# Kernel tuning notes

Hardware: AMD Instinct MI355X
Metric: run time of the kernel (lower is better)

The kernel has to match this reference:

```python
import jax, jax.numpy as jnp
import numpy as np

B, D, R = 4096, 1024, 256
DT = 0.01
DT_SCALE = 1.0

# Yoshida 4th-order coefficients
_W1 = 1.0 / (2.0 - 2.0 ** (1.0 / 3.0))
_W0 = -(2.0 ** (1.0 / 3.0)) / (2.0 - 2.0 ** (1.0 / 3.0))
C1 = _W1 / 2.0
C2 = (_W0 + _W1) / 2.0
C3 = C2
C4 = C1
D1 = _W1
D2 = _W0
D3 = _W1


def setup_inputs() -> dict:
    key = jax.random.key(0)
    k1, k2, k3, k4, k5 = jax.random.split(key, 5)
    x = jax.random.normal(k1, (B, D), dtype=jnp.float32)
    v = jax.random.normal(k2, (B, D), dtype=jnp.float32)
    force = jax.random.normal(k3, (B, D), dtype=jnp.float32)
    # low-rank christoffel factors, scaled for numerical stability
    U = jax.random.normal(k4, (R, D), dtype=jnp.float32) * (1.0 / np.sqrt(D))
    W = jax.random.normal(k5, (D, R), dtype=jnp.float32) * (1.0 / np.sqrt(R))
    return {"x": x, "v": v, "force": force, "U": U, "W": W}


def _christoffel(tv, tx, U, W):
    # Gamma(v) = W @ (U v)^2  (low-rank quadratic form; x unused, matching
    # the gfn yoshida_fused(U, W) signature)
    h = jnp.einsum("rd,bd->br", U, tv)  # [B, R]
    return jnp.einsum("dr,br->bd", W, h * h)  # [B, D]


def reference(x, v, force, U, W):
    dt = DT * DT_SCALE

    def acceleration(tx, tv):
        return -_christoffel(tv, tx, U, W) + force

    x1 = x + C1 * dt * v
    v1 = v + D1 * dt * acceleration(x1, v)
    x2 = x1 + C2 * dt * v1
    v2 = v1 + D2 * dt * acceleration(x2, v1)
    x3 = x2 + C3 * dt * v2
    v3 = v2 + D3 * dt * acceleration(x3, v2)
    x_final = x3 + C4 * dt * v3
    return (x_final, v3)
```

## Files before the change

### kernel.cpp

```cpp
#include <hip/hip_runtime.h>
#include <hip/hip_bf16.h>


#define BSZ 4096
#define DD 1024
#define RR 256

typedef unsigned short ushort_t;
typedef __attribute__((ext_vector_type(8))) short short8;
typedef __attribute__((ext_vector_type(4))) float f32x4;

__device__ inline ushort_t f2b(float x) {
    union { float f; unsigned int u; } c;
    c.f = x;
    unsigned int lsb = (c.u >> 16) & 1u;
    return (ushort_t)((c.u + 0x7fffu + lsb) >> 16);
}

__global__ __launch_bounds__(256) void pack_uw_kernel(
    const float* __restrict__ U, const float* __restrict__ W,
    ushort_t* __restrict__ Upk, ushort_t* __restrict__ Wpk)
{
    const int g = blockIdx.x * 256 + threadIdx.x;
    const float* src;
    ushort_t* dst;
    if (g < 32768) {
        const int l = g & 63;
        const int kt = (g >> 6) & 31, nt = g >> 11;
        src = U + (size_t)(nt * 16 + (l & 15)) * DD + kt * 32 + (l >> 4) * 8;
        dst = Upk + (size_t)g * 8;
    } else {
        const int g2 = g - 32768;
        const int l = g2 & 63;
        const int kt = (g2 >> 6) & 7, dtile = g2 >> 9;
        src = W + (size_t)(dtile * 16 + (l & 15)) * RR + kt * 32 + (l >> 4) * 8;
        dst = Wpk + (size_t)g2 * 8;
    }
    const float4 a = *reinterpret_cast<const float4*>(src);
    const float4 b = *reinterpret_cast<const float4*>(src + 4);
    ushort_t t[8] = {f2b(a.x), f2b(a.y), f2b(a.z), f2b(a.w),
                     f2b(b.x), f2b(b.y), f2b(b.z), f2b(b.w)};
    *reinterpret_cast<short8*>(dst) = *reinterpret_cast<short8*>(t);
}

__global__ __launch_bounds__(1024) void yoshida_fused_kernel(
    const float* __restrict__ x_in,
    const float* __restrict__ v_in,
    const float* __restrict__ force,
    const ushort_t* __restrict__ Upk,
    const ushort_t* __restrict__ Wpk,
    float* __restrict__ x_out,
    float* __restrict__ v_out)
{
    __shared__ __align__(16) ushort_t vS[16][1032];
    __shared__ __align__(16) ushort_t H2S[16][264];

    const int tid = threadIdx.x;
    const int w = tid >> 6;
    const int l = tid & 63;
    const int m = l & 15;
    const int q = l >> 4;
    const int b0 = blockIdx.x * 16;
    const int d0 = w * 64;

    constexpr double CBRT2 = 1.2599210498948731647672106072782;
    constexpr double W1c = 1.0 / (2.0 - CBRT2);
    constexpr double W0c = -CBRT2 * W1c;
    constexpr double DTd = 0.01 * 1.0;
    const float dcoef[3] = {(float)(W1c * DTd), (float)(W0c * DTd), (float)(W1c * DTd)};
    const float xcoef[3] = {(float)((W0c + W1c) * 0.5), (float)((W0c + W1c) * 0.5),
                            (float)(W1c * 0.5)};
    const float c1  = (float)(W1c * 0.5);
    const float dtf = (float)DTd;

    float vreg[16], xacc[16], freg[16];
    #pragma unroll
    for (int t = 0; t < 4; ++t)
        #pragma unroll
        for (int i = 0; i < 4; ++i) {
            const size_t gidx = (size_t)(b0 + q * 4 + i) * DD + d0 + t * 16 + m;
            const float vv = v_in[gidx];
            vreg[t * 4 + i] = vv;
            xacc[t * 4 + i] = c1 * vv;
            freg[t * 4 + i] = force[gidx];
        }

    {
        const int row = tid >> 6;
        const int col = (tid & 63) * 16;
        const float* sp = v_in + (size_t)(b0 + row) * DD + col;
        const float4 f0 = *reinterpret_cast<const float4*>(sp);
        const float4 f1 = *reinterpret_cast<const float4*>(sp + 4);
        const float4 f2 = *reinterpret_cast<const float4*>(sp + 8);
        const float4 f3 = *reinterpret_cast<const float4*>(sp + 12);
        ushort_t tmp[16] = {f2b(f0.x), f2b(f0.y), f2b(f0.z), f2b(f0.w),
                            f2b(f1.x), f2b(f1.y), f2b(f1.z), f2b(f1.w),
                            f2b(f2.x), f2b(f2.y), f2b(f2.z), f2b(f2.w),
                            f2b(f3.x), f2b(f3.y), f2b(f3.z), f2b(f3.w)};
        *reinterpret_cast<short8*>(&vS[row][col])     = *reinterpret_cast<short8*>(&tmp[0]);
        *reinterpret_cast<short8*>(&vS[row][col + 8]) = *reinterpret_cast<short8*>(&tmp[8]);
    }

    const ushort_t* up = Upk + (size_t)(w * 16384 + l * 8);
    const ushort_t* wp = Wpk + (size_t)(w * 16384 + l * 8);

    short8 ub[4];
    #pragma unroll
    for (int p = 0; p < 4; ++p)
        ub[p] = *reinterpret_cast<const short8*>(up + (size_t)p * 512);

    #pragma unroll
    for (int s = 0; s < 3; ++s) {
        __syncthreads();

        f32x4 a0 = {0.f, 0.f, 0.f, 0.f}, a1 = {0.f, 0.f, 0.f, 0.f};
        #pragma unroll
        for (int kt = 0; kt < 32; ++kt) {
            const short8 b = ub[kt & 3];
            if (kt < 28)
                ub[kt & 3] = *reinterpret_cast<const short8*>(up + (size_t)(kt + 4) * 512);
            const short8 a = *reinterpret_cast<const short8*>(&vS[m][kt * 32 + q * 8]);
            if (kt & 1) a1 = __builtin_amdgcn_mfma_f32_16x16x32_bf16(a, b, a1, 0, 0, 0);
            else        a0 = __builtin_amdgcn_mfma_f32_16x16x32_bf16(a, b, a0, 0, 0, 0);
        }
        #pragma unroll
        for (int i = 0; i < 4; ++i) {
            const float h = a0[i] + a1[i];
            H2S[q * 4 + i][w * 16 + m] = f2b(h * h);
        }

        short8 wb[4];
        #pragma unroll
        for (int t = 0; t < 4; ++t)
            wb[t] = *reinterpret_cast<const short8*>(wp + (size_t)(t * 8) * 512);
        __syncthreads();

        f32x4 accB[4];
        #pragma unroll
        for (int t = 0; t < 4; ++t) accB[t] = (f32x4){0.f, 0.f, 0.f, 0.f};
        #pragma unroll
        for (int kt = 0; kt < 8; ++kt) {
            const short8 a = *reinterpret_cast<const short8*>(&H2S[m][kt * 32 + q * 8]);
            #pragma unroll
            for (int t = 0; t < 4; ++t) {
                const short8 b = wb[t];
                if (kt < 7)
                    wb[t] = *reinterpret_cast<const short8*>(wp + (size_t)(t * 8 + kt + 1) * 512);
                accB[t] = __builtin_amdgcn_mfma_f32_16x16x32_bf16(a, b, accB[t], 0, 0, 0);
            }
        }

        const float ddt = dcoef[s], cx = xcoef[s];
        #pragma unroll
        for (int t = 0; t < 4; ++t)
            #pragma unroll
            for (int i = 0; i < 4; ++i) {
                const float vn = vreg[t * 4 + i] + ddt * (freg[t * 4 + i] - accB[t][i]);
                vreg[t * 4 + i] = vn;
                xacc[t * 4 + i] += cx * vn;
                vS[q * 4 + i][d0 + t * 16 + m] = f2b(vn);
            }

        if (s < 2) {
            #pragma unroll
            for (int p = 0; p < 4; ++p)
                ub[p] = *reinterpret_cast<const short8*>(up + (size_t)p * 512);
        }
    }

    #pragma unroll
    for (int t = 0; t < 4; ++t)
        #pragma unroll
        for (int i = 0; i < 4; ++i) {
            const size_t g = (size_t)(b0 + q * 4 + i) * DD + d0 + t * 16 + m;
            x_out[g] = x_in[g] + dtf * xacc[t * 4 + i];
            v_out[g] = vreg[t * 4 + i];
        }
}

extern "C" void kernel_launch(void* const* d_in, const int* in_sizes, int n_in,
                              void* d_out, int out_size, void* d_ws, size_t ws_size,
                              hipStream_t stream) {
    const float* x     = (const float*)d_in[0];
    const float* v     = (const float*)d_in[1];
    const float* force = (const float*)d_in[2];
    const float* U     = (const float*)d_in[3];
    const float* W     = (const float*)d_in[4];

    float* x_out = (float*)d_out;
    float* v_out = x_out + (size_t)BSZ * DD;

    ushort_t* Upk = (ushort_t*)d_ws;
    ushort_t* Wpk = Upk + (size_t)RR * DD;

    pack_uw_kernel<<<dim3(256), dim3(256), 0, stream>>>(U, W, Upk, Wpk);
    yoshida_fused_kernel<<<dim3(BSZ / 16), dim3(1024), 0, stream>>>(
        x, v, force, Upk, Wpk, x_out, v_out);
}
```

Baseline: 137.9 us.

## Switch low-rank Christoffel GEMMs from bf16 to fp8 MFMA with scaling

Both GEMMs inside the Yoshida steps now use fp8 operands and the 16x16x32 fp8 MFMA instead of bf16. U and W are packed to fp8 with power-of-two prescales, and the factors are undone in the squared activations and the velocity update. This halves weight bytes and shared-memory traffic, and the register-prefetch pipelining of weight loads is dropped in favour of direct 16-byte loads per step. The cost is much lower precision for v, h^2 and the weights, which risks exceeding the accuracy tolerance.

New measurement: 132.8 us. 3.7% less time.

```diff
diff --git a/kernel.cpp b/kernel.cpp
--- a/kernel.cpp
+++ b/kernel.cpp
@@ -1,65 +1,72 @@
 #include <hip/hip_runtime.h>
-#include <hip/hip_bf16.h>
 
 
 #define BSZ 4096
 #define DD 1024
 #define RR 256
 
-typedef unsigned short ushort_t;
-typedef __attribute__((ext_vector_type(8))) short short8;
+typedef unsigned char uchar;
+typedef long long i64;
+typedef __attribute__((ext_vector_type(2))) long i64x2;
 typedef __attribute__((ext_vector_type(4))) float f32x4;
+typedef __attribute__((ext_vector_type(4))) unsigned int uint4v;
 
-__device__ inline ushort_t f2b(float x) {
-    union { float f; unsigned int u; } c;
-    c.f = x;
-    unsigned int lsb = (c.u >> 16) & 1u;
-    return (ushort_t)((c.u + 0x7fffu + lsb) >> 16);
+__device__ inline unsigned int f2q4(float a, float b, float c, float d) {
+    int lo = __builtin_amdgcn_cvt_pk_fp8_f32(a, b, 0, false);
+    int hi = __builtin_amdgcn_cvt_pk_fp8_f32(c, d, lo, true);
+    return (unsigned int)hi;
+}
+__device__ inline uchar f2q1(float x) {
+    return (uchar)(__builtin_amdgcn_cvt_pk_fp8_f32(x, x, 0, false) & 0xff);
 }
 
 __global__ __launch_bounds__(256) void pack_uw_kernel(
     const float* __restrict__ U, const float* __restrict__ W,
-    ushort_t* __restrict__ Upk, ushort_t* __restrict__ Wpk)
+    uchar* __restrict__ Upk, uchar* __restrict__ Wpk)
 {
     const int g = blockIdx.x * 256 + threadIdx.x;
     const float* src;
-    ushort_t* dst;
-    if (g < 32768) {
-        const int l = g & 63;
-        const int kt = (g >> 6) & 31, nt = g >> 11;
-        src = U + (size_t)(nt * 16 + (l & 15)) * DD + kt * 32 + (l >> 4) * 8;
-        dst = Upk + (size_t)g * 8;
+    uchar* dst;
+    float sc;
+    if (g < 16384) {
+        const int l = g & 63, p = (g >> 6) & 15, nt = g >> 10;
+        src = U + (size_t)(nt * 16 + (l & 15)) * DD + p * 64 + (l >> 4) * 8;
+        dst = Upk + ((size_t)nt << 14) + (p << 10) + (l << 4);
+        sc = 8.0f;
     } else {
-        const int g2 = g - 32768;
-        const int l = g2 & 63;
-        const int kt = (g2 >> 6) & 7, dtile = g2 >> 9;
-        src = W + (size_t)(dtile * 16 + (l & 15)) * RR + kt * 32 + (l >> 4) * 8;
-        dst = Wpk + (size_t)g2 * 8;
+        const int g2 = g - 16384;
+        const int l = g2 & 63, p = (g2 >> 6) & 3, dt_ = g2 >> 8;
+        src = W + (size_t)(dt_ * 16 + (l & 15)) * RR + p * 64 + (l >> 4) * 8;
+        dst = Wpk + ((size_t)dt_ << 12) + (p << 10) + (l << 4);
+        sc = 16.0f;
     }
-    const float4 a = *reinterpret_cast<const float4*>(src);
-    const float4 b = *reinterpret_cast<const float4*>(src + 4);
-    ushort_t t[8] = {f2b(a.x), f2b(a.y), f2b(a.z), f2b(a.w),
-                     f2b(b.x), f2b(b.y), f2b(b.z), f2b(b.w)};
-    *reinterpret_cast<short8*>(dst) = *reinterpret_cast<short8*>(t);
+    const float4 x0 = *reinterpret_cast<const float4*>(src);
+    const float4 x1 = *reinterpret_cast<const float4*>(src + 4);
+    const float4 y0 = *reinterpret_cast<const float4*>(src + 32);
+    const float4 y1 = *reinterpret_cast<const float4*>(src + 36);
+    uint4v o;
+    o.x = f2q4(sc * x0.x, sc * x0.y, sc * x0.z, sc * x0.w);
+    o.y = f2q4(sc * x1.x, sc * x1.y, sc * x1.z, sc * x1.w);
+    o.z = f2q4(sc * y0.x, sc * y0.y, sc * y0.z, sc * y0.w);
+    o.w = f2q4(sc * y1.x, sc * y1.y, sc * y1.z, sc * y1.w);
+    *reinterpret_cast<uint4v*>(dst) = o;
 }
 
 __global__ __launch_bounds__(1024) void yoshida_fused_kernel(
     const float* __restrict__ x_in,
     const float* __restrict__ v_in,
     const float* __restrict__ force,
-    const ushort_t* __restrict__ Upk,
-    const ushort_t* __restrict__ Wpk,
+    const uchar* __restrict__ Upk,
+    const uchar* __restrict__ Wpk,
     float* __restrict__ x_out,
     float* __restrict__ v_out)
 {
-    __shared__ __align__(16) ushort_t vS[16][1032];
-    __shared__ __align__(16) ushort_t H2S[16][264];
+    __shared__ __align__(16) uchar vS[16][1040];
+    __shared__ __align__(16) uchar H2S[16][272];
 
     const int tid = threadIdx.x;
-    const int w = tid >> 6;
-    const int l = tid & 63;
-    const int m = l & 15;
-    const int q = l >> 4;
+    const int w = tid >> 6, l = tid & 63;
+    const int m = l & 15, q = l >> 4;
     const int b0 = blockIdx.x * 16;
     const int d0 = w * 64;
 
@@ -93,21 +100,16 @@
         const float4 f1 = *reinterpret_cast<const float4*>(sp + 4);
         const float4 f2 = *reinterpret_cast<const float4*>(sp + 8);
         const float4 f3 = *reinterpret_cast<const float4*>(sp + 12);
-        ushort_t tmp[16] = {f2b(f0.x), f2b(f0.y), f2b(f0.z), f2b(f0.w),
-                            f2b(f1.x), f2b(f1.y), f2b(f1.z), f2b(f1.w),
-                            f2b(f2.x), f2b(f2.y), f2b(f2.z), f2b(f2.w),
-                            f2b(f3.x), f2b(f3.y), f2b(f3.z), f2b(f3.w)};
-        *reinterpret_cast<short8*>(&vS[row][col])     = *reinterpret_cast<short8*>(&tmp[0]);
-        *reinterpret_cast<short8*>(&vS[row][col + 8]) = *reinterpret_cast<short8*>(&tmp[8]);
+        uint4v pk;
+        pk.x = f2q4(f0.x, f0.y, f0.z, f0.w);
+        pk.y = f2q4(f1.x, f1.y, f1.z, f1.w);
+        pk.z = f2q4(f2.x, f2.y, f2.z, f2.w);
+        pk.w = f2q4(f3.x, f3.y, f3.z, f3.w);
+        *reinterpret_cast<uint4v*>(&vS[row][col]) = pk;
     }
 
-    const ushort_t* up = Upk + (size_t)(w * 16384 + l * 8);
-    const ushort_t* wp = Wpk + (size_t)(w * 16384 + l * 8);
-
-    short8 ub[4];
-    #pragma unroll
-    for (int p = 0; p < 4; ++p)
-        ub[p] = *reinterpret_cast<const short8*>(up + (size_t)p * 512);
+    const uchar* up = Upk + ((size_t)w << 14) + (l << 4);
+    const uchar* wp = Wpk + ((size_t)(w * 4) << 12) + (l << 4);
 
     #pragma unroll
     for (int s = 0; s < 3; ++s) {
@@ -115,57 +117,46 @@
 
         f32x4 a0 = {0.f, 0.f, 0.f, 0.f}, a1 = {0.f, 0.f, 0.f, 0.f};
         #pragma unroll
-        for (int kt = 0; kt < 32; ++kt) {
-            const short8 b = ub[kt & 3];
-            if (kt < 28)
-                ub[kt & 3] = *reinterpret_cast<const short8*>(up + (size_t)(kt + 4) * 512);
-            const short8 a = *reinterpret_cast<const short8*>(&vS[m][kt * 32 + q * 8]);
-            if (kt & 1) a1 = __builtin_amdgcn_mfma_f32_16x16x32_bf16(a, b, a1, 0, 0, 0);
-            else        a0 = __builtin_amdgcn_mfma_f32_16x16x32_bf16(a, b, a0, 0, 0, 0);
+        for (int p = 0; p < 16; ++p) {
+            const i64x2 bb = *reinterpret_cast<const i64x2*>(up + (p << 10));
+            const i64 af0 = *reinterpret_cast<const i64*>(&vS[m][p * 64 + q * 8]);
+            const i64 af1 = *reinterpret_cast<const i64*>(&vS[m][p * 64 + 32 + q * 8]);
+            a0 = __builtin_amdgcn_mfma_f32_16x16x32_fp8_fp8(af0, bb.x, a0, 0, 0, 0);
+            a1 = __builtin_amdgcn_mfma_f32_16x16x32_fp8_fp8(af1, bb.y, a1, 0, 0, 0);
         }
         #pragma unroll
         for (int i = 0; i < 4; ++i) {
-            const float h = a0[i] + a1[i];
-            H2S[q * 4 + i][w * 16 + m] = f2b(h * h);
+            const float h8 = a0[i] + a1[i];
+            H2S[q * 4 + i][w * 16 + m] = f2q1(h8 * h8 * 0.015625f);
         }
-
-        short8 wb[4];
-        #pragma unroll
-        for (int t = 0; t < 4; ++t)
-            wb[t] = *reinterpret_cast<const short8*>(wp + (size_t)(t * 8) * 512);
         __syncthreads();
 
         f32x4 accB[4];
         #pragma unroll
         for (int t = 0; t < 4; ++t) accB[t] = (f32x4){0.f, 0.f, 0.f, 0.f};
         #pragma unroll
-        for (int kt = 0; kt < 8; ++kt) {
-            const short8 a = *reinterpret_cast<const short8*>(&H2S[m][kt * 32 + q * 8]);
+        for (int p = 0; p < 4; ++p) {
+            const i64 ha0 = *reinterpret_cast<const i64*>(&H2S[m][p * 64 + q * 8]);
+            const i64 ha1 = *reinterpret_cast<const i64*>(&H2S[m][p * 64 + 32 + q * 8]);
             #pragma unroll
             for (int t = 0; t < 4; ++t) {
-                const short8 b = wb[t];
-                if (kt < 7)
-                    wb[t] = *reinterpret_cast<const short8*>(wp + (size_t)(t * 8 + kt + 1) * 512);
-                accB[t] = __builtin_amdgcn_mfma_f32_16x16x32_bf16(a, b, accB[t], 0, 0, 0);
+                const i64x2 wb = *reinterpret_cast<const i64x2*>(wp + (t << 12) + (p << 10));
+                accB[t] = __builtin_amdgcn_mfma_f32_16x16x32_fp8_fp8(ha0, wb.x, accB[t], 0, 0, 0);
+                accB[t] = __builtin_amdgcn_mfma_f32_16x16x32_fp8_fp8(ha1, wb.y, accB[t], 0, 0, 0);
             }
         }
 
-        const float ddt = dcoef[s], cx = xcoef[s];
+        const float ddt = dcoef[s], cx = xcoef[s], gsc = dcoef[s] * 0.0625f;
         #pragma unroll
         for (int t = 0; t < 4; ++t)
             #pragma unroll
             for (int i = 0; i < 4; ++i) {
-                const float vn = vreg[t * 4 + i] + ddt * (freg[t * 4 + i] - accB[t][i]);
+                const float vn = vreg[t * 4 + i] + ddt * freg[t * 4 + i]
+                                 - gsc * accB[t][i];
                 vreg[t * 4 + i] = vn;
                 xacc[t * 4 + i] += cx * vn;
-                vS[q * 4 + i][d0 + t * 16 + m] = f2b(vn);
+                vS[q * 4 + i][d0 + t * 16 + m] = f2q1(vn);
             }
-
-        if (s < 2) {
-            #pragma unroll
-            for (int p = 0; p < 4; ++p)
-                ub[p] = *reinterpret_cast<const short8*>(up + (size_t)p * 512);
-        }
     }
 
     #pragma unroll
@@ -190,10 +181,10 @@
     float* x_out = (float*)d_out;
     float* v_out = x_out + (size_t)BSZ * DD;
 
-    ushort_t* Upk = (ushort_t*)d_ws;
-    ushort_t* Wpk = Upk + (size_t)RR * DD;
+    uchar* Upk = (uchar*)d_ws;
+    uchar* Wpk = Upk + (size_t)RR * DD;
 
-    pack_uw_kernel<<<dim3(256), dim3(256), 0, stream>>>(U, W, Upk, Wpk);
+    pack_uw_kernel<<<dim3(128), dim3(256), 0, stream>>>(U, W, Upk, Wpk);
     yoshida_fused_kernel<<<dim3(BSZ / 16), dim3(1024), 0, stream>>>(
         x, v, force, Upk, Wpk, x_out, v_out);
 }
```
